# Optimization experiments

Hardware: AMD Instinct MI355X
Metric: run time of the kernel (lower is better)

The kernel has to match this reference:

```python
import jax, jax.numpy as jnp
import numpy as np


def _lstm(x, Wx, Wh, b):
    """Fused-gate LSTM over time axis 1. x: [B,T,I]; Wx: [I,4H]; Wh: [H,4H]; b: [4H].
    Gate order (i, f, g, o) as in flax.linen.LSTMCell. Zero initial carry."""
    B, T, _ = x.shape
    H = Wh.shape[0]
    # Precompute all input-to-gate contributions in one big GEMM.
    xg = jnp.einsum('bti,ih->bth', x, Wx) + b  # [B,T,4H]

    def step(carry, xt):
        c, h = carry
        z = xt + h @ Wh  # [B,4H]
        i, f, g, o = jnp.split(z, 4, axis=-1)
        c = jax.nn.sigmoid(f) * c + jax.nn.sigmoid(i) * jnp.tanh(g)
        h = jax.nn.sigmoid(o) * jnp.tanh(c)
        return (c, h), h

    init = (jnp.zeros((B, H), x.dtype), jnp.zeros((B, H), x.dtype))
    _, hs = jax.lax.scan(step, init, jnp.swapaxes(xg, 0, 1))  # hs: [T,B,H]
    return jnp.swapaxes(hs, 0, 1)  # [B,T,H]


def _forward(X, conv_w, conv_b,
             Wx1, Wh1, b1, Wx2, Wh2, b2, Wx3, Wh3, b3, Wx4, Wh4, b4,
             Wa, ba, Va, bva, Wd1, bd1, Wd2, bd2):
    # 1-D conv, SAME padding (flax default), NWC layout.
    x = jax.lax.conv_general_dilated(X, conv_w, (1,), 'SAME',
                                     dimension_numbers=('NWC', 'WIO', 'NWC')) + conv_b
    # NOTE: source uses jnp.flip(..., axis=-1) -> flips FEATURE axis (faithful to source).
    x1 = _lstm(x, Wx1, Wh1, b1)
    x2 = _lstm(jnp.flip(x, axis=-1), Wx2, Wh2, b2)
    x = jnp.concatenate([x1, x2], axis=-1)  # [B,T,2F]
    x1 = _lstm(x, Wx3, Wh3, b3)
    x2 = _lstm(jnp.flip(x, axis=-1), Wx4, Wh4, b4)
    enc = jnp.concatenate([x1, x2], axis=-1)  # [B,T,4F]
    # Additive attention: softmax over time axis.
    score = jnp.tanh(enc @ Wa + ba) @ Va + bva  # [B,T,1]
    w = jax.nn.softmax(score, axis=1)
    ctx = jnp.sum(w * enc, axis=1)  # [B,4F]
    # MLP head (dropout deterministic -> identity).
    h = jnp.tanh(ctx @ Wd1 + bd1)
    return h @ Wd2 + bd2  # [B,1]


def setup_inputs() -> dict:
    key = jax.random.key(0)
    B, T, Cin, F = 32, 4096, 8, 64
    ks = iter(jax.random.split(key, 32))

    def w(shape):
        fan_in = shape[0] if len(shape) <= 2 else shape[0] * shape[1]
        return jax.random.normal(next(ks), shape, jnp.float32) / np.sqrt(fan_in)

    d = {}
    d['X'] = jax.random.normal(next(ks), (B, T, Cin), jnp.float32)
    d['conv_w'] = w((4, Cin, 16))
    d['conv_b'] = jnp.zeros((16,), jnp.float32)
    lstm_dims = {'1': (16, F), '2': (16, F), '3': (2 * F, 2 * F), '4': (2 * F, 2 * F)}
    for n, (i_dim, h_dim) in lstm_dims.items():
        d['Wx' + n] = w((i_dim, 4 * h_dim))
        d['Wh' + n] = w((h_dim, 4 * h_dim))
        d['b' + n] = jnp.zeros((4 * h_dim,), jnp.float32)
    d['Wa'] = w((4 * F, F)); d['ba'] = jnp.zeros((F,), jnp.float32)
    d['Va'] = w((F, 1));     d['bva'] = jnp.zeros((1,), jnp.float32)
    d['Wd1'] = w((4 * F, F)); d['bd1'] = jnp.zeros((F,), jnp.float32)
    d['Wd2'] = w((F, 1));     d['bd2'] = jnp.zeros((1,), jnp.float32)
    d['deterministic'] = 1
    return d


def reference(X, conv_w, conv_b,
              Wx1, Wh1, b1, Wx2, Wh2, b2, Wx3, Wh3, b3, Wx4, Wh4, b4,
              Wa, ba, Va, bva, Wd1, bd1, Wd2, bd2, deterministic):
    # deterministic=1 -> dropout is the identity; already reflected in _forward.
    return _forward(X, conv_w, conv_b,
                    Wx1, Wh1, b1, Wx2, Wh2, b2, Wx3, Wh3, b3, Wx4, Wh4, b4,
                    Wa, ba, Va, bva, Wd1, bd1, Wd2, bd2)
```

## Files before the change

kernel.cpp:

```cpp
#include <hip/hip_runtime.h>


#define TFULL 4096
#define NB 32

__device__ __forceinline__ float fexp2(float x){ return __builtin_amdgcn_exp2f(x); }
__device__ __forceinline__ float frcp(float x){ return __builtin_amdgcn_rcpf(x); }
__device__ __forceinline__ float sigf(float x){ return frcp(1.f + fexp2(-1.44269504f*x)); }
__device__ __forceinline__ float tanh_(float x){
    float e = fexp2(fminf(2.88539008f*x, 126.f));
    return (e - 1.f) * frcp(e + 1.f);
}
#define PIN4(v) asm volatile("" : "+v"(v.x), "+v"(v.y), "+v"(v.z), "+v"(v.w))

__global__ __launch_bounds__(256) void k_init(float* __restrict__ st1,
        float* __restrict__ st2, float* __restrict__ am, float* __restrict__ al,
        float* __restrict__ acc){
    int i = blockIdx.x * 256 + threadIdx.x;
    if (i < 8192)  st1[i] = 0.f;
    if (i < 16384) st2[i] = 0.f;
    if (i < 8192)  acc[i] = 0.f;
    if (i < 32){ am[i] = -3.4e38f; al[i] = 0.f; }
}

__global__ __launch_bounds__(256) void k_pack(
        const float* __restrict__ Wx1, const float* __restrict__ Wh1, const float* __restrict__ b1,
        const float* __restrict__ Wx2, const float* __restrict__ Wh2, const float* __restrict__ b2,
        const float* __restrict__ Wx3, const float* __restrict__ Wh3, const float* __restrict__ b3,
        const float* __restrict__ Wx4, const float* __restrict__ Wh4, const float* __restrict__ b4,
        float* __restrict__ W34, float* __restrict__ b34, float* __restrict__ W2p,
        float* __restrict__ W1p, float* __restrict__ b12){
    int i0 = blockIdx.x * 256 + threadIdx.x;
    int stride = gridDim.x * 256;
    for (int e = i0; e < 131072; e += stride){
        int k = e >> 10, n = e & 1023;
        W34[e] = (n < 512) ? Wx3[k*512 + n] : Wx4[(127 - k)*512 + (n - 512)];
    }
    for (int e = i0; e < 1024; e += stride) b34[e] = (e < 512) ? b3[e] : b4[e - 512];
    for (int e = i0; e < 131072; e += stride){
        int l = e >> 16, f = e & 65535;
        int p = f >> 14, g = f & 16383, tid = g >> 5, kk = g & 31;
        int q = tid & 127, s = tid >> 7;
        W2p[e] = (l ? Wh4 : Wh3)[(32*s + kk)*512 + 4*q + p];
    }
    for (int e = i0; e < 65536; e += stride){
        int l = e >> 15, r = e & 32767, tid = r >> 6, wq = r & 63;
        int q = tid & 63, s = tid >> 6;
        float v = 0.f;
        if (wq < 32){
            int c = wq >> 3, k = wq & 7;
            v = (l ? Wh2 : Wh1)[(s*8 + k)*256 + (4*q + c)];
        } else if (s < 2){
            int c = (wq - 32) >> 3, rr = (wq - 32) & 7;
            int rg = s*8 + rr, col = 4*q + c;
            v = l ? Wx2[(15 - rg)*256 + col] : Wx1[rg*256 + col];
        }
        W1p[e] = v;
    }
    for (int e = i0; e < 512; e += stride) b12[e] = (e < 256) ? b1[e] : b2[e - 256];
}

__global__ __launch_bounds__(256) void k_conv(const float* __restrict__ X,
        const float* __restrict__ W, const float* __restrict__ Bv,
        float* __restrict__ out, int t0, int lc){
    __shared__ float Ws[512];
    __shared__ float bs[16];
    int tid = threadIdx.x;
    Ws[tid] = W[tid]; Ws[tid + 256] = W[tid + 256];
    if (tid < 16) bs[tid] = Bv[tid];
    __syncthreads();
    int m = blockIdx.x * 256 + tid;
    int b = m >> lc, trel = m & ((1 << lc) - 1);
    int t = t0 + trel;
    float o[16];
    #pragma unroll
    for (int co = 0; co < 16; ++co) o[co] = bs[co];
    #pragma unroll
    for (int w = 0; w < 4; ++w){
        int tt = t + w - 1;
        if (tt >= 0 && tt < TFULL){
            const float* xr = X + ((size_t)(b << 12) + tt) * 8;
            #pragma unroll
            for (int ci = 0; ci < 8; ++ci){
                float v = xr[ci];
                #pragma unroll
                for (int co = 0; co < 16; ++co) o[co] += v * Ws[(w*8 + ci)*16 + co];
            }
        }
    }
    float* op = out + (size_t)m * 16;
    #pragma unroll
    for (int q = 0; q < 4; ++q)
        *(float4*)(op + q*4) = make_float4(o[q*4], o[q*4+1], o[q*4+2], o[q*4+3]);
}

__global__ void __launch_bounds__(512, 1)
k_scan1(const float* __restrict__ x, const float* __restrict__ W1p,
        const float* __restrict__ b12,
        float* __restrict__ cc, float* __restrict__ st1, int C){
    int l = blockIdx.x >> 5;
    int b = blockIdx.x & 31;
    int tid = threadIdx.x;
    int q = tid & 63;
    int s = tid >> 6;
    float4 w[16];
    {
        const float4* wp = (const float4*)(W1p + ((size_t)l*512 + tid)*64);
        #pragma unroll
        for (int i = 0; i < 16; ++i) w[i] = wp[i];
        #pragma unroll
        for (int i = 0; i < 16; ++i) PIN4(w[i]);
    }
    float bi0 = 0.f, bi1 = 0.f, bi2 = 0.f, bi3 = 0.f;
    if (tid < 64){
        bi0 = b12[l*256 + tid];       bi1 = b12[l*256 + 64 + tid];
        bi2 = b12[l*256 + 128 + tid]; bi3 = b12[l*256 + 192 + tid];
    }

    __shared__ float xs[128 * 16];
    __shared__ float zp[8 * 256];
    __shared__ float hbufs[64];
    float c = 0.f;
    int sidx = (l*32 + b)*64 + (tid & 63);
    if (tid < 64){ c = st1[sidx]; hbufs[tid] = st1[4096 + sidx]; }
    __syncthreads();

    const float* xb = x + ((size_t)b * C) * 16;
    float* ccb = cc + ((size_t)b * C) * 128 + (l << 6);

    #pragma clang loop unroll(disable)
    for (int t = 0; t < C; ++t){
        int st = t & 127;
        if (st == 0){
            __syncthreads();
            const float4* src = (const float4*)(xb + (size_t)t * 16);
            float4* dst = (float4*)xs;
            if (t + (tid >> 2) < C) dst[tid] = src[tid];
            __syncthreads();
        }
        float a0 = 0.f, a1 = 0.f, a2 = 0.f, a3 = 0.f;
        const float4* hb4 = (const float4*)hbufs + (s << 1);
        #pragma unroll
        for (int k4 = 0; k4 < 2; ++k4){
            float4 hv = hb4[k4];
            a0 = fmaf(hv.x, w[k4].x, a0);     a0 = fmaf(hv.y, w[k4].y, a0);
            a0 = fmaf(hv.z, w[k4].z, a0);     a0 = fmaf(hv.w, w[k4].w, a0);
            a1 = fmaf(hv.x, w[2+k4].x, a1);   a1 = fmaf(hv.y, w[2+k4].y, a1);
            a1 = fmaf(hv.z, w[2+k4].z, a1);   a1 = fmaf(hv.w, w[2+k4].w, a1);
            a2 = fmaf(hv.x, w[4+k4].x, a2);   a2 = fmaf(hv.y, w[4+k4].y, a2);
            a2 = fmaf(hv.z, w[4+k4].z, a2);   a2 = fmaf(hv.w, w[4+k4].w, a2);
            a3 = fmaf(hv.x, w[6+k4].x, a3);   a3 = fmaf(hv.y, w[6+k4].y, a3);
            a3 = fmaf(hv.z, w[6+k4].z, a3);   a3 = fmaf(hv.w, w[6+k4].w, a3);
        }
        if (s < 2){
            const float4* xr = (const float4*)(xs + st * 16) + (s << 1);
            #pragma unroll
            for (int r4 = 0; r4 < 2; ++r4){
                float4 xv = xr[r4];
                a0 = fmaf(xv.x, w[8+r4].x, a0);    a0 = fmaf(xv.y, w[8+r4].y, a0);
                a0 = fmaf(xv.z, w[8+r4].z, a0);    a0 = fmaf(xv.w, w[8+r4].w, a0);
                a1 = fmaf(xv.x, w[10+r4].x, a1);   a1 = fmaf(xv.y, w[10+r4].y, a1);
                a1 = fmaf(xv.z, w[10+r4].z, a1);   a1 = fmaf(xv.w, w[10+r4].w, a1);
                a2 = fmaf(xv.x, w[12+r4].x, a2);   a2 = fmaf(xv.y, w[12+r4].y, a2);
                a2 = fmaf(xv.z, w[12+r4].z, a2);   a2 = fmaf(xv.w, w[12+r4].w, a2);
                a3 = fmaf(xv.x, w[14+r4].x, a3);   a3 = fmaf(xv.y, w[14+r4].y, a3);
                a3 = fmaf(xv.w, w[14+r4].w, a3);   a3 = fmaf(xv.z, w[14+r4].z, a3);
            }
        }
        *(float4*)(zp + (s << 8) + (q << 2)) = make_float4(a0, a1, a2, a3);
        __syncthreads();
        if (tid < 64){
            float zi = bi0, zf = bi1, zg = bi2, zo = bi3;
            #pragma unroll
            for (int ss = 0; ss < 8; ++ss){
                const float* zr = zp + (ss << 8);
                zi += zr[tid]; zf += zr[64 + tid]; zg += zr[128 + tid]; zo += zr[192 + tid];
            }
            c = sigf(zf) * c + sigf(zi) * tanh_(zg);
            float h = sigf(zo) * tanh_(c);
            hbufs[tid] = h;
            ccb[(size_t)t * 128 + tid] = h;
        }
        __syncthreads();
    }
    if (tid < 64){ st1[sidx] = c; st1[4096 + sidx] = hbufs[tid]; }
}

template<bool TANH>
__global__ __launch_bounds__(128) void k_gemm(
        const float* __restrict__ A, int lda,
        const float* __restrict__ B, int ldb,
        const float* __restrict__ bias,
        float* __restrict__ Cm, int ldc, int K){
    __shared__ float As[64 * 129];
    __shared__ float Bs[64 * 68];
    int tid = threadIdx.x;
    int tx = tid & 7;
    int ty = tid >> 3;
    int r0 = blockIdx.x * 128;
    int n0 = blockIdx.y * 64;
    float acc[8][8];
    #pragma unroll
    for (int i = 0; i < 8; ++i)
        #pragma unroll
        for (int n = 0; n < 8; ++n) acc[i][n] = 0.f;

    for (int kb = 0; kb < K; kb += 64){
        __syncthreads();
        for (int idx = tid; idx < 2048; idx += 128){
            int r = idx >> 4, k4 = idx & 15;
            float4 v = *(const float4*)(A + (size_t)(r0 + r) * lda + kb + k4*4);
            As[(k4*4 + 0)*129 + r] = v.x;
            As[(k4*4 + 1)*129 + r] = v.y;
            As[(k4*4 + 2)*129 + r] = v.z;
            As[(k4*4 + 3)*129 + r] = v.w;
        }
        for (int idx = tid; idx < 1024; idx += 128){
            int n4 = idx & 15, k = idx >> 4;
            float4 v = *(const float4*)(B + (size_t)(kb + k) * ldb + n0 + n4*4);
            *(float4*)(Bs + k*68 + n4*4) = v;
        }
        __syncthreads();
        #pragma unroll 4
        for (int k = 0; k < 64; ++k){
            float a[8];
            #pragma unroll
            for (int i = 0; i < 8; ++i) a[i] = As[k*129 + ty*8 + i];
            float4 b0 = *(const float4*)(Bs + k*68 + tx*8);
            float4 b1 = *(const float4*)(Bs + k*68 + tx*8 + 4);
            float bq[8] = {b0.x, b0.y, b0.z, b0.w, b1.x, b1.y, b1.z, b1.w};
            #pragma unroll
            for (int i = 0; i < 8; ++i)
                #pragma unroll
                for (int n = 0; n < 8; ++n) acc[i][n] += a[i] * bq[n];
        }
    }
    #pragma unroll
    for (int i = 0; i < 8; ++i){
        size_t rr = (size_t)r0 + ty*8 + i;
        float* cp = Cm + rr * ldc + n0 + tx*8;
        float ov[8];
        #pragma unroll
        for (int n = 0; n < 8; ++n){
            float v = acc[i][n] + bias[n0 + tx*8 + n];
            ov[n] = TANH ? tanh_(v) : v;
        }
        *(float4*)cp       = make_float4(ov[0], ov[1], ov[2], ov[3]);
        *(float4*)(cp + 4) = make_float4(ov[4], ov[5], ov[6], ov[7]);
    }
}

__global__ void __launch_bounds__(512, 1)
k_scan2(const float* __restrict__ xg, const float* __restrict__ W2p,
        float* __restrict__ enc, float* __restrict__ st2, int C){
    int l = blockIdx.x >> 5;
    int b = blockIdx.x & 31;
    int tid = threadIdx.x;
    int q = tid & 127;
    int s = tid >> 7;

    __shared__ float smem[16384 + 128];
    float* zp = smem;
    float* hbufs = smem + 16384;

    float c = 0.f;
    int sidx = (l*32 + b)*128 + (tid & 127);
    if (tid < 128){ c = st2[sidx]; hbufs[tid] = st2[8192 + sidx]; }

    float4 w[32];
    const float* Wg = W2p + (size_t)l * 65536;
    for (int p = 0; p < 4; ++p){
        __syncthreads();
        const float4* src4 = (const float4*)(Wg + p * 16384);
        float4* dst4 = (float4*)smem;
        #pragma unroll
        for (int v = 0; v < 8; ++v) dst4[v*512 + tid] = src4[v*512 + tid];
        __syncthreads();
        const float4* ws4 = (const float4*)smem + tid*8;
        #pragma unroll
        for (int j = 0; j < 8; ++j) w[p*8 + j] = ws4[j];
    }
    #pragma unroll
    for (int i = 0; i < 32; ++i) PIN4(w[i]);
    __syncthreads();

    const float4* xp4 = (const float4*)(xg + ((size_t)b * C) * 1024 + (l << 9)) + q;
    float* encb = enc + ((size_t)b * C) * 256 + (l << 7);

    float4 xn = make_float4(0.f, 0.f, 0.f, 0.f);
    if (s == 0) xn = xp4[0];
    #pragma clang loop unroll(disable)
    for (int t = 0; t < C; ++t){
        float a0, a1, a2, a3;
        if (s == 0){
            a0 = xn.x; a1 = xn.y; a2 = xn.z; a3 = xn.w;
            int tn = (t + 1 < C) ? t + 1 : t;
            xn = xp4[(size_t)tn * 256];
        } else { a0 = a1 = a2 = a3 = 0.f; }
        const float4* hb4 = (const float4*)hbufs + (s << 3);
        #pragma unroll
        for (int k4 = 0; k4 < 8; ++k4){
            float4 hv = hb4[k4];
            a0 = fmaf(hv.x, w[k4].x, a0);      a0 = fmaf(hv.y, w[k4].y, a0);
            a0 = fmaf(hv.z, w[k4].z, a0);      a0 = fmaf(hv.w, w[k4].w, a0);
            a1 = fmaf(hv.x, w[8+k4].x, a1);    a1 = fmaf(hv.y, w[8+k4].y, a1);
            a1 = fmaf(hv.z, w[8+k4].z, a1);    a1 = fmaf(hv.w, w[8+k4].w, a1);
            a2 = fmaf(hv.x, w[16+k4].x, a2);   a2 = fmaf(hv.y, w[16+k4].y, a2);
            a2 = fmaf(hv.z, w[16+k4].z, a2);   a2 = fmaf(hv.w, w[16+k4].w, a2);
            a3 = fmaf(hv.x, w[24+k4].x, a3);   a3 = fmaf(hv.y, w[24+k4].y, a3);
            a3 = fmaf(hv.z, w[24+k4].z, a3);   a3 = fmaf(hv.w, w[24+k4].w, a3);
        }
        *(float4*)(zp + (s << 9) + (q << 2)) = make_float4(a0, a1, a2, a3);
        __syncthreads();
        if (tid < 128){
            float zi = zp[tid]       + zp[512 + tid]  + zp[1024 + tid] + zp[1536 + tid];
            float zf = zp[128 + tid] + zp[640 + tid]  + zp[1152 + tid] + zp[1664 + tid];
            float zg = zp[256 + tid] + zp[768 + tid]  + zp[1280 + tid] + zp[1792 + tid];
            float zo = zp[384 + tid] + zp[896 + tid]  + zp[1408 + tid] + zp[1920 + tid];
            c = sigf(zf) * c + sigf(zi) * tanh_(zg);
            float h = sigf(zo) * tanh_(c);
            hbufs[tid] = h;
            encb[(size_t)t * 256 + tid] = h;
        }
        __syncthreads();
    }
    if (tid < 128){ st2[sidx] = c; st2[8192 + sidx] = hbufs[tid]; }
}

__global__ __launch_bounds__(256) void k_scorev(const float* __restrict__ u,
        const float* __restrict__ Va, const float* __restrict__ bva,
        float* __restrict__ sc){
    int m = blockIdx.x * 256 + threadIdx.x;
    const float4* up = (const float4*)(u + (size_t)m * 64);
    const float4* vp = (const float4*)Va;
    float acc = 0.f;
    #pragma unroll
    for (int i = 0; i < 16; ++i){
        float4 v = up[i], w = vp[i];
        acc += v.x*w.x + v.y*w.y + v.z*w.z + v.w*w.w;
    }
    sc[m] = acc + bva[0];
}

__global__ __launch_bounds__(1024) void k_attn(const float* __restrict__ sc,
        const float* __restrict__ enc, float* __restrict__ am,
        float* __restrict__ al, float* __restrict__ acc, int C){
    int b = blockIdx.x, tid = threadIdx.x;
    __shared__ float es[1024];
    __shared__ float red[16];
    __shared__ float sh[2];
    const float* sp = sc + (size_t)b * C;
    float mloc = -3.4e38f;
    for (int t = tid; t < C; t += 1024) mloc = fmaxf(mloc, sp[t]);
    #pragma unroll
    for (int off = 32; off; off >>= 1) mloc = fmaxf(mloc, __shfl_down(mloc, off));
    if ((tid & 63) == 0) red[tid >> 6] = mloc;
    __syncthreads();
    if (tid == 0){
        float mc = -3.4e38f;
        #pragma unroll
        for (int i = 0; i < 16; ++i) mc = fmaxf(mc, red[i]);
        float mo = am[b];
        float mn = fmaxf(mo, mc);
        sh[0] = mn;
        sh[1] = fexp2(1.44269504f * (mo - mn));
        am[b] = mn;
    }
    __syncthreads();
    float mn = sh[0], alpha = sh[1];
    float eloc = 0.f;
    for (int t = tid; t < C; t += 1024){
        float e = fexp2(1.44269504f * (sp[t] - mn));
        es[t] = e; eloc += e;
    }
    #pragma unroll
    for (int off = 32; off; off >>= 1) eloc += __shfl_down(eloc, off);
    if ((tid & 63) == 0) red[tid >> 6] = eloc;
    __syncthreads();
    if (tid == 0){
        float sm = 0.f;
        #pragma unroll
        for (int i = 0; i < 16; ++i) sm += red[i];
        al[b] = al[b] * alpha + sm;
    }
    int jf = tid & 255, sl = tid >> 8;
    int tlen = C >> 2;
    const float* ep = enc + ((size_t)b * C + (size_t)sl * tlen) * 256 + jf;
    const float* eb = es + sl * tlen;
    float a = 0.f;
    for (int t = 0; t < tlen; ++t) a = fmaf(eb[t], ep[(size_t)t * 256], a);
    __syncthreads();
    es[tid] = a;
    __syncthreads();
    if (tid < 256)
        acc[b*256 + tid] = acc[b*256 + tid] * alpha
                         + ((es[tid] + es[256 + tid]) + (es[512 + tid] + es[768 + tid]));
}

__global__ __launch_bounds__(256) void k_head(const float* __restrict__ acc,
        const float* __restrict__ al,
        const float* __restrict__ Wd1, const float* __restrict__ bd1,
        const float* __restrict__ Wd2, const float* __restrict__ bd2,
        float* __restrict__ out){
    __shared__ float ctxs[32 * 256];
    __shared__ float h1s[32 * 64];
    int tid = threadIdx.x;
    for (int idx = tid; idx < 8192; idx += 256){
        int b = idx >> 8;
        ctxs[idx] = acc[idx] / al[b];
    }
    __syncthreads();
    for (int idx = tid; idx < 2048; idx += 256){
        int b = idx >> 6, n = idx & 63;
        float a = bd1[n];
        for (int i = 0; i < 256; ++i) a += ctxs[b*256 + i] * Wd1[i*64 + n];
        h1s[idx] = tanh_(a);
    }
    __syncthreads();
    if (tid < 32){
        float a = bd2[0];
        #pragma unroll
        for (int n = 0; n < 64; ++n) a += h1s[tid*64 + n] * Wd2[n];
        out[tid] = a;
    }
}

extern "C" void kernel_launch(void* const* d_in, const int* in_sizes, int n_in,
                              void* d_out, int out_size, void* d_ws, size_t ws_size,
                              hipStream_t stream){
    const float* X     = (const float*)d_in[0];
    const float* convw = (const float*)d_in[1];
    const float* convb = (const float*)d_in[2];
    const float* Wx1 = (const float*)d_in[3];
    const float* Wh1 = (const float*)d_in[4];
    const float* b1  = (const float*)d_in[5];
    const float* Wx2 = (const float*)d_in[6];
    const float* Wh2 = (const float*)d_in[7];
    const float* b2  = (const float*)d_in[8];
    const float* Wx3 = (const float*)d_in[9];
    const float* Wh3 = (const float*)d_in[10];
    const float* b3  = (const float*)d_in[11];
    const float* Wx4 = (const float*)d_in[12];
    const float* Wh4 = (const float*)d_in[13];
    const float* b4  = (const float*)d_in[14];
    const float* Wa  = (const float*)d_in[15];
    const float* ba  = (const float*)d_in[16];
    const float* Va  = (const float*)d_in[17];
    const float* bva = (const float*)d_in[18];
    const float* Wd1 = (const float*)d_in[19];
    const float* bd1 = (const float*)d_in[20];
    const float* Wd2 = (const float*)d_in[21];
    const float* bd2 = (const float*)d_in[22];
    float* out = (float*)d_out;
    (void)in_sizes; (void)n_in; (void)out_size;

    const size_t fixedFl = 131072 + 1024 + 131072 + 65536 + 512
                         + 8192 + 16384 + 32 + 32 + 8192 + 32*1024;
    size_t capFl = ws_size / 4;
    int C = 1024;
    while (C > 32){
        size_t need = fixedFl + (size_t)NB * C * (16 + 128 + 1024 + 256 + 64);
        if (need <= capFl) break;
        C >>= 1;
    }
    int lc = 31 - __builtin_clz((unsigned)C);
    int nch = TFULL / C;

    float* ws   = (float*)d_ws;
    float* W34  = ws;
    float* b34  = W34 + 131072;
    float* W2p  = b34 + 1024;
    float* W1p  = W2p + 131072;
    float* b12  = W1p + 65536;
    float* st1  = b12 + 512;
    float* st2  = st1 + 8192;
    float* am   = st2 + 16384;
    float* al   = am + 32;
    float* acc  = al + 32;
    float* scb  = acc + 8192;
    float* xcv  = scb + 32*1024;
    float* ccb  = xcv + (size_t)NB*C*16;
    float* xgb  = ccb + (size_t)NB*C*128;
    float* enb  = xgb + (size_t)NB*C*1024;
    float* ub   = enb + (size_t)NB*C*256;

    k_init<<<64, 256, 0, stream>>>(st1, st2, am, al, acc);
    k_pack<<<512, 256, 0, stream>>>(Wx1, Wh1, b1, Wx2, Wh2, b2,
                                    Wx3, Wh3, b3, Wx4, Wh4, b4,
                                    W34, b34, W2p, W1p, b12);

    for (int ch = 0; ch < nch; ++ch){
        int t0 = ch * C;
        k_conv<<<NB*C/256, 256, 0, stream>>>(X, convw, convb, xcv, t0, lc);
        k_scan1<<<64, 512, 0, stream>>>(xcv, W1p, b12, ccb, st1, C);
        k_gemm<false><<<dim3(NB*C/128, 16), 128, 0, stream>>>(
            ccb, 128, W34, 1024, b34, xgb, 1024, 128);
        k_scan2<<<64, 512, 0, stream>>>(xgb, W2p, enb, st2, C);
        k_gemm<true><<<dim3(NB*C/128, 1), 128, 0, stream>>>(
            enb, 256, Wa, 64, ba, ub, 64, 256);
        k_scorev<<<NB*C/256, 256, 0, stream>>>(ub, Va, bva, scb);
        k_attn<<<32, 1024, 0, stream>>>(scb, enb, am, al, acc, C);
    }
    k_head<<<1, 256, 0, stream>>>(acc, al, Wd1, bd1, Wd2, bd2, out);
}
```

Measured before the change: 5.897 ms.

## Stage LSTM hidden outputs and input gates in shared memory, flush in batches

```diff
diff --git a/kernel.cpp b/kernel.cpp
--- a/kernel.cpp
+++ b/kernel.cpp
@@ -119,23 +119,32 @@
 
     __shared__ float xs[128 * 16];
     __shared__ float zp[8 * 256];
+    __shared__ float ccbuf[128 * 64];
     __shared__ float hbufs[64];
     float c = 0.f;
-    int sidx = (l*32 + b)*64 + (tid & 63);
+    int sidx = (l*32 + b)*64 + q;
     if (tid < 64){ c = st1[sidx]; hbufs[tid] = st1[4096 + sidx]; }
     __syncthreads();
 
     const float* xb = x + ((size_t)b * C) * 16;
     float* ccb = cc + ((size_t)b * C) * 128 + (l << 6);
+    int BS = C < 128 ? C : 128;
+    int bsm = BS - 1;
+    int fr = tid >> 2, fi = tid & 3;
 
     #pragma clang loop unroll(disable)
     for (int t = 0; t < C; ++t){
-        int st = t & 127;
+        int st = t & bsm;
         if (st == 0){
             __syncthreads();
-            const float4* src = (const float4*)(xb + (size_t)t * 16);
-            float4* dst = (float4*)xs;
-            if (t + (tid >> 2) < C) dst[tid] = src[tid];
+            if (t && fr < BS){
+                const float4* cb4 = (const float4*)ccbuf + fr*16 + fi*4;
+                float4* cgp = (float4*)(ccb + (size_t)(t - BS + fr)*128) + fi*4;
+                #pragma unroll
+                for (int i = 0; i < 4; ++i) cgp[i] = cb4[i];
+            }
+            if (tid < BS*4)
+                ((float4*)xs)[tid] = ((const float4*)(xb + (size_t)t*16))[tid];
             __syncthreads();
         }
         float a0 = 0.f, a1 = 0.f, a2 = 0.f, a3 = 0.f;
@@ -164,7 +173,7 @@
                 a2 = fmaf(xv.x, w[12+r4].x, a2);   a2 = fmaf(xv.y, w[12+r4].y, a2);
                 a2 = fmaf(xv.z, w[12+r4].z, a2);   a2 = fmaf(xv.w, w[12+r4].w, a2);
                 a3 = fmaf(xv.x, w[14+r4].x, a3);   a3 = fmaf(xv.y, w[14+r4].y, a3);
-                a3 = fmaf(xv.w, w[14+r4].w, a3);   a3 = fmaf(xv.z, w[14+r4].z, a3);
+                a3 = fmaf(xv.z, w[14+r4].z, a3);   a3 = fmaf(xv.w, w[14+r4].w, a3);
             }
         }
         *(float4*)(zp + (s << 8) + (q << 2)) = make_float4(a0, a1, a2, a3);
@@ -179,9 +188,15 @@
             c = sigf(zf) * c + sigf(zi) * tanh_(zg);
             float h = sigf(zo) * tanh_(c);
             hbufs[tid] = h;
-            ccb[(size_t)t * 128 + tid] = h;
-        }
-        __syncthreads();
+            ccbuf[st*64 + tid] = h;
+        }
+        __syncthreads();
+    }
+    if (fr < BS){
+        const float4* cb4 = (const float4*)ccbuf + fr*16 + fi*4;
+        float4* cgp = (float4*)(ccb + (size_t)(C - BS + fr)*128) + fi*4;
+        #pragma unroll
+        for (int i = 0; i < 4; ++i) cgp[i] = cb4[i];
     }
     if (tid < 64){ st1[sidx] = c; st1[4096 + sidx] = hbufs[tid]; }
 }
@@ -259,12 +274,14 @@
     int q = tid & 127;
     int s = tid >> 7;
 
-    __shared__ float smem[16384 + 128];
-    float* zp = smem;
-    float* hbufs = smem + 16384;
+    __shared__ float smem[16384 + 4096 + 2048 + 128];
+    float* xgbuf  = smem;
+    float* encbuf = smem + 16384;
+    float* zp     = smem + 20480;
+    float* hbufs  = smem + 22528;
 
     float c = 0.f;
-    int sidx = (l*32 + b)*128 + (tid & 127);
+    int sidx = (l*32 + b)*128 + q;
     if (tid < 128){ c = st2[sidx]; hbufs[tid] = st2[8192 + sidx]; }
 
     float4 w[32];
@@ -272,30 +289,46 @@
     for (int p = 0; p < 4; ++p){
         __syncthreads();
         const float4* src4 = (const float4*)(Wg + p * 16384);
-        float4* dst4 = (float4*)smem;
+        float4* dst4 = (float4*)xgbuf;
         #pragma unroll
         for (int v = 0; v < 8; ++v) dst4[v*512 + tid] = src4[v*512 + tid];
         __syncthreads();
-        const float4* ws4 = (const float4*)smem + tid*8;
+        const float4* ws4 = (const float4*)xgbuf + tid*8;
         #pragma unroll
         for (int j = 0; j < 8; ++j) w[p*8 + j] = ws4[j];
     }
     #pragma unroll
     for (int i = 0; i < 32; ++i) PIN4(w[i]);
-    __syncthreads();
-
-    const float4* xp4 = (const float4*)(xg + ((size_t)b * C) * 1024 + (l << 9)) + q;
+
+    const float* xgg = xg + ((size_t)b * C) * 1024 + (l << 9);
     float* encb = enc + ((size_t)b * C) * 256 + (l << 7);
-
-    float4 xn = make_float4(0.f, 0.f, 0.f, 0.f);
-    if (s == 0) xn = xp4[0];
+    int tq = tid & 15, tr = tid >> 4;
+
     #pragma clang loop unroll(disable)
     for (int t = 0; t < C; ++t){
+        int st = t & 31;
+        if (st == 0){
+            __syncthreads();
+            if (t){
+                const float4* eb4 = (const float4*)encbuf + tr*32;
+                float* eg = encb + (size_t)(t - 32 + tr) * 256;
+                #pragma unroll
+                for (int i = 0; i < 2; ++i)
+                    *(float4*)(eg + (tq + i*16)*4) = eb4[tq + i*16];
+            }
+            {
+                const float4* xs4 = (const float4*)(xgg + (size_t)(t + tr) * 1024);
+                float4* xb4 = (float4*)xgbuf + tr*128;
+                #pragma unroll
+                for (int i = 0; i < 8; ++i)
+                    xb4[tq + i*16] = xs4[tq + i*16];
+            }
+            __syncthreads();
+        }
         float a0, a1, a2, a3;
         if (s == 0){
-            a0 = xn.x; a1 = xn.y; a2 = xn.z; a3 = xn.w;
-            int tn = (t + 1 < C) ? t + 1 : t;
-            xn = xp4[(size_t)tn * 256];
+            float4 xv = *((const float4*)(xgbuf + st*512) + q);
+            a0 = xv.x; a1 = xv.y; a2 = xv.z; a3 = xv.w;
         } else { a0 = a1 = a2 = a3 = 0.f; }
         const float4* hb4 = (const float4*)hbufs + (s << 3);
         #pragma unroll
@@ -320,9 +353,16 @@
             c = sigf(zf) * c + sigf(zi) * tanh_(zg);
             float h = sigf(zo) * tanh_(c);
             hbufs[tid] = h;
-            encb[(size_t)t * 256 + tid] = h;
-        }
-        __syncthreads();
+            encbuf[st*128 + tid] = h;
+        }
+        __syncthreads();
+    }
+    {
+        const float4* eb4 = (const float4*)encbuf + tr*32;
+        float* eg = encb + (size_t)(C - 32 + tr) * 256;
+        #pragma unroll
+        for (int i = 0; i < 2; ++i)
+            *(float4*)(eg + (tq + i*16)*4) = eb4[tq + i*16];
     }
     if (tid < 128){ st2[sidx] = c; st2[8192 + sidx] = hbufs[tid]; }
 }
```

After: 5.783 ms. Within noise of the previous version (-1.9%).
